# Optimization experiments

Measured on AMD Instinct MI355X. Metric: run time of the kernel, lower is better.

## Reference

```python
import jax, jax.numpy as jnp
import numpy as np

B, H, S, DK = 4, 16, 1024, 64


def setup_inputs() -> dict:
    key = jax.random.key(0)
    kq, kk, kv, km = jax.random.split(key, 4)
    q = jax.random.normal(kq, (B, H, S, DK), dtype=jnp.float32)
    k = jax.random.normal(kk, (B, H, S, DK), dtype=jnp.float32)
    v = jax.random.normal(kv, (B, H, S, DK), dtype=jnp.float32)
    mask = jax.random.randint(km, (B, 1, 1, S), 0, 2).astype(jnp.int32)
    return {"q": q, "k": k, "v": v, "mask": mask}


def reference(q, k, v, mask):
    dk = q.shape[-1]
    scale = 1.0 / np.sqrt(dk).astype(np.float32)
    # [B,H,S,S] scores
    qk = jnp.einsum("bhqd,bhkd->bhqk", q, k) * scale
    qk = jnp.where(mask == 0, jnp.float32(-10000.0), qk)
    attn_weight = jax.nn.softmax(qk, axis=-1)
    # NOTE: faithful to source bug — uses raw masked scores qk, not attn_weight
    output = jnp.einsum("bhqk,bhkd->bhqd", qk, v)
    return (output, attn_weight)
```

## Files before the change

### kernel.cpp

```cpp
#include <hip/hip_runtime.h>


typedef __attribute__((ext_vector_type(4))) float floatx4;
typedef __attribute__((ext_vector_type(8))) short shortx8;
typedef __attribute__((ext_vector_type(8))) unsigned short ushortx8;
typedef __attribute__((ext_vector_type(4))) int intx4;

#define S_ 1024
#define D_ 64
#define NELEM_ 4194304
#define ATTN_OFF 4194304
#define SCN 1040

__device__ __forceinline__ unsigned short f32_to_bf16(float f) {
    union { float f; unsigned u; } a; a.f = f;
    unsigned u = a.u;
    u += 0x7fffu + ((u >> 16) & 1u);
    return (unsigned short)(u >> 16);
}

__device__ __forceinline__ float bf16_to_f32(unsigned short h) {
    union { unsigned u; float f; } a; a.u = ((unsigned)h) << 16;
    return a.f;
}

__device__ __forceinline__ ushortx8 pack8u(floatx4 a, floatx4 b) {
    ushortx8 r;
    r[0] = f32_to_bf16(a[0]); r[1] = f32_to_bf16(a[1]);
    r[2] = f32_to_bf16(a[2]); r[3] = f32_to_bf16(a[3]);
    r[4] = f32_to_bf16(b[0]); r[5] = f32_to_bf16(b[1]);
    r[6] = f32_to_bf16(b[2]); r[7] = f32_to_bf16(b[3]);
    return r;
}

__global__ __launch_bounds__(256) void pack_kv(const float* __restrict__ k,
                                               const float* __restrict__ v,
                                               unsigned short* __restrict__ kbt,
                                               unsigned short* __restrict__ vtp) {
    __shared__ float tile[64][65];
    if (blockIdx.x < 1024) {
        int g = blockIdx.x * 256 + threadIdx.x;
        int lane = g & 63;
        int kt   = (g >> 6) & 63;
        int bh   = g >> 12;
        int quad = lane >> 4;
        int l15  = lane & 15;
        const float* src = k + ((size_t)(bh * S_ + kt * 16 + l15)) * D_ + quad * 8;
        floatx4 f0 = *(const floatx4*)(src);
        floatx4 f1 = *(const floatx4*)(src + 4);
        floatx4 f2 = *(const floatx4*)(src + 32);
        floatx4 f3 = *(const floatx4*)(src + 36);
        unsigned short* dst = kbt + (size_t)g * 16;
        *(ushortx8*)(dst)     = pack8u(f0, f1);
        *(ushortx8*)(dst + 8) = pack8u(f2, f3);
    } else {
        int blk = blockIdx.x - 1024;
        int bh = blk >> 4;
        int s0 = (blk & 15) << 6;
        int tid = threadIdx.x;
        int r  = tid >> 2;
        int c0 = (tid & 3) << 4;
        const float* src = v + ((size_t)(bh * S_ + s0 + r)) * D_ + c0;
        #pragma unroll
        for (int j = 0; j < 4; ++j) {
            floatx4 f = *(const floatx4*)(src + j * 4);
            tile[r][c0 + j*4 + 0] = f[0];
            tile[r][c0 + j*4 + 1] = f[1];
            tile[r][c0 + j*4 + 2] = f[2];
            tile[r][c0 + j*4 + 3] = f[3];
        }
        __syncthreads();
        int d  = tid >> 2;
        int so = (tid & 3) << 4;
        int dt  = d >> 4;
        int l15 = d & 15;
        ushortx8 h0, h1;
        #pragma unroll
        for (int j = 0; j < 8; ++j) h0[j] = f32_to_bf16(tile[so + j][d]);
        #pragma unroll
        for (int j = 0; j < 8; ++j) h1[j] = f32_to_bf16(tile[so + 8 + j][d]);
        int sA = s0 + so;
        int ksA = sA >> 5, qA = (sA & 31) >> 3;
        int sB = sA + 8;
        int ksB = sB >> 5, qB = (sB & 31) >> 3;
        size_t baseA = ((((size_t)bh * 4 + dt) * 32 + ksA) * 64 + qA * 16 + l15) * 8;
        size_t baseB = ((((size_t)bh * 4 + dt) * 32 + ksB) * 64 + qB * 16 + l15) * 8;
        *(ushortx8*)(vtp + baseA) = h0;
        *(ushortx8*)(vtp + baseB) = h1;
    }
}

__global__ __launch_bounds__(1024, 4) void attn_main(
    const float* __restrict__ q,
    const int* __restrict__ mask,
    const unsigned short* __restrict__ KbT,
    const unsigned short* __restrict__ VtP,
    float* __restrict__ out)
{
    __shared__ unsigned short sc[64 * SCN];
    __shared__ int msk[1024];

    int blk = blockIdx.x;
    int bh  = blk >> 4;
    int q0  = (blk & 15) << 6;
    int b   = bh >> 4;
    int tid = threadIdx.x;

    msk[tid] = mask[(b << 10) + tid];

    int w    = tid >> 6;
    int lane = tid & 63;
    int l15  = lane & 15;
    int quad = lane >> 4;
    int rg   = w & 3;
    int cg   = w >> 2;

    shortx8 qf0, qf1;
    {
        const float* qb = q + ((size_t)(bh * S_ + q0 + rg * 16 + l15)) * D_ + quad * 8;
        floatx4 a0 = *(const floatx4*)(qb);
        floatx4 a1 = *(const floatx4*)(qb + 4);
        floatx4 b0 = *(const floatx4*)(qb + 32);
        floatx4 b1 = *(const floatx4*)(qb + 36);
        ushortx8 u0 = pack8u(a0, a1);
        ushortx8 u1 = pack8u(b0, b1);
        qf0 = (shortx8)u0;
        qf1 = (shortx8)u1;
    }

    __syncthreads();

    {
        const unsigned short* kb = KbT + ((size_t)bh * 64 * 64 + lane) * 16;
        #pragma unroll 4
        for (int t = 0; t < 16; ++t) {
            int kt = (cg << 4) + t;
            const unsigned short* p = kb + (size_t)kt * (64 * 16);
            shortx8 kf0 = *(const shortx8*)(p);
            shortx8 kf1 = *(const shortx8*)(p + 8);
            floatx4 acc = {0.f, 0.f, 0.f, 0.f};
            acc = __builtin_amdgcn_mfma_f32_16x16x32_bf16(qf0, kf0, acc, 0, 0, 0);
            acc = __builtin_amdgcn_mfma_f32_16x16x32_bf16(qf1, kf1, acc, 0, 0, 0);
            int n0 = kt << 4;
            int mv = msk[n0 + l15];
            int col = n0 + l15;
            #pragma unroll
            for (int r = 0; r < 4; ++r) {
                unsigned short h = mv ? f32_to_bf16(acc[r] * 0.125f)
                                      : (unsigned short)0xC61C;
                sc[(rg * 16 + quad * 4 + r) * SCN + col] = h;
            }
        }
    }
    __syncthreads();

    auto phase2 = [&]() {
        float* attnb = out + ATTN_OFF + ((size_t)(bh * S_ + q0)) * S_;
        for (int rr = 0; rr < 4; ++rr) {
            int row = (w << 2) + rr;
            const unsigned short* srow = sc + row * SCN;
            float vv[16];
            #pragma unroll
            for (int c = 0; c < 2; ++c) {
                ushortx8 h = *(const ushortx8*)(srow + (c << 9) + lane * 8);
                #pragma unroll
                for (int j = 0; j < 8; ++j) vv[c * 8 + j] = bf16_to_f32(h[j]);
            }
            float m = vv[0];
            #pragma unroll
            for (int j = 1; j < 16; ++j) m = fmaxf(m, vv[j]);
            #pragma unroll
            for (int off = 32; off; off >>= 1) m = fmaxf(m, __shfl_xor(m, off));
            float s = 0.f;
            #pragma unroll
            for (int j = 0; j < 16; ++j) { vv[j] = __expf(vv[j] - m); s += vv[j]; }
            #pragma unroll
            for (int off = 32; off; off >>= 1) s += __shfl_xor(s, off);
            float inv = 1.0f / s;
            float* arow = attnb + (size_t)row * S_ + lane * 8;
            #pragma unroll
            for (int c = 0; c < 2; ++c) {
                floatx4 o0 = { vv[c*8+0]*inv, vv[c*8+1]*inv, vv[c*8+2]*inv, vv[c*8+3]*inv };
                floatx4 o1 = { vv[c*8+4]*inv, vv[c*8+5]*inv, vv[c*8+6]*inv, vv[c*8+7]*inv };
                *(floatx4*)(arow + (c << 9))     = o0;
                *(floatx4*)(arow + (c << 9) + 4) = o1;
            }
        }
    };
    auto phase3 = [&]() {
        const unsigned short* vb = VtP + (((size_t)bh * 4 + cg) * 32) * (64 * 8) + lane * 8;
        const unsigned short* sr = sc + (rg * 16 + l15) * SCN + quad * 8;
        floatx4 oacc = {0.f, 0.f, 0.f, 0.f};
        #pragma unroll 4
        for (int ks = 0; ks < 32; ++ks) {
            shortx8 af = *(const shortx8*)(sr + (ks << 5));
            shortx8 bf = *(const shortx8*)(vb + (ks << 9));
            oacc = __builtin_amdgcn_mfma_f32_16x16x32_bf16(af, bf, oacc, 0, 0, 0);
        }
        float* ob = out + ((size_t)(bh * S_ + q0 + rg * 16 + (quad << 2))) * D_
                        + (cg << 4) + l15;
        #pragma unroll
        for (int r = 0; r < 4; ++r) ob[(size_t)r * D_] = oacc[r];
    };
    if (w & 1) { phase3(); phase2(); }
    else       { phase2(); phase3(); }
}

extern "C" void kernel_launch(void* const* d_in, const int* in_sizes, int n_in,
                              void* d_out, int out_size, void* d_ws, size_t ws_size,
                              hipStream_t stream) {
    const float* q   = (const float*)d_in[0];
    const float* k   = (const float*)d_in[1];
    const float* v   = (const float*)d_in[2];
    const int* mask  = (const int*)d_in[3];
    float* out = (float*)d_out;
    unsigned short* KbT = (unsigned short*)d_ws;
    unsigned short* VtP = KbT + NELEM_;
    pack_kv<<<2048, 256, 0, stream>>>(k, v, KbT, VtP);
    attn_main<<<1024, 1024, 0, stream>>>(q, mask, KbT, VtP, out);
}
```

Before: 369.3 us.

## Reassign waves: register-blocked QK/PV tiles, dedicated softmax and PV waves, block swizzle

Each wave now holds all four Q row-group fragments and computes a 64x64 score block per K tile, so every K fragment load is reused across four MFMAs. The PV phase is handled by four dedicated waves that each reuse one V fragment across four row groups, while the other twelve waves do the softmax and attention-weight writes (6 or 5 rows each) instead of every wave doing both phases. It also pads the score row stride to change LDS bank mapping and swizzles the block index so consecutive blocks land on different heads. The costs are higher register pressure from the fragment and accumulator arrays, and an uneven split of work between the softmax waves and the PV waves.

Measured after the change: 387.6 us. +5.0%, slower.

```diff
diff --git a/kernel.cpp b/kernel.cpp
--- a/kernel.cpp
+++ b/kernel.cpp
@@ -4,13 +4,13 @@
 typedef __attribute__((ext_vector_type(4))) float floatx4;
 typedef __attribute__((ext_vector_type(8))) short shortx8;
 typedef __attribute__((ext_vector_type(8))) unsigned short ushortx8;
-typedef __attribute__((ext_vector_type(4))) int intx4;
 
 #define S_ 1024
 #define D_ 64
 #define NELEM_ 4194304
 #define ATTN_OFF 4194304
-#define SCN 1040
+#define SCN 1048
+#define QT 64
 
 __device__ __forceinline__ unsigned short f32_to_bf16(float f) {
     union { float f; unsigned u; } a; a.f = f;
@@ -97,10 +97,10 @@
     const unsigned short* __restrict__ VtP,
     float* __restrict__ out)
 {
-    __shared__ unsigned short sc[64 * SCN];
+    __shared__ unsigned short sc[QT * SCN];
     __shared__ int msk[1024];
 
-    int blk = blockIdx.x;
+    int blk = ((blockIdx.x & 7) << 7) | (blockIdx.x >> 3);
     int bh  = blk >> 4;
     int q0  = (blk & 15) << 6;
     int b   = bh >> 4;
@@ -112,52 +112,58 @@
     int lane = tid & 63;
     int l15  = lane & 15;
     int quad = lane >> 4;
-    int rg   = w & 3;
-    int cg   = w >> 2;
-
-    shortx8 qf0, qf1;
-    {
+
+    shortx8 qf0[4], qf1[4];
+    #pragma unroll
+    for (int rg = 0; rg < 4; ++rg) {
         const float* qb = q + ((size_t)(bh * S_ + q0 + rg * 16 + l15)) * D_ + quad * 8;
         floatx4 a0 = *(const floatx4*)(qb);
         floatx4 a1 = *(const floatx4*)(qb + 4);
-        floatx4 b0 = *(const floatx4*)(qb + 32);
-        floatx4 b1 = *(const floatx4*)(qb + 36);
-        ushortx8 u0 = pack8u(a0, a1);
-        ushortx8 u1 = pack8u(b0, b1);
-        qf0 = (shortx8)u0;
-        qf1 = (shortx8)u1;
+        floatx4 a2 = *(const floatx4*)(qb + 32);
+        floatx4 a3 = *(const floatx4*)(qb + 36);
+        qf0[rg] = (shortx8)pack8u(a0, a1);
+        qf1[rg] = (shortx8)pack8u(a2, a3);
     }
 
     __syncthreads();
 
     {
         const unsigned short* kb = KbT + ((size_t)bh * 64 * 64 + lane) * 16;
-        #pragma unroll 4
-        for (int t = 0; t < 16; ++t) {
-            int kt = (cg << 4) + t;
+        #pragma unroll
+        for (int t = 0; t < 4; ++t) {
+            int kt = (w << 2) + t;
             const unsigned short* p = kb + (size_t)kt * (64 * 16);
             shortx8 kf0 = *(const shortx8*)(p);
             shortx8 kf1 = *(const shortx8*)(p + 8);
-            floatx4 acc = {0.f, 0.f, 0.f, 0.f};
-            acc = __builtin_amdgcn_mfma_f32_16x16x32_bf16(qf0, kf0, acc, 0, 0, 0);
-            acc = __builtin_amdgcn_mfma_f32_16x16x32_bf16(qf1, kf1, acc, 0, 0, 0);
+            floatx4 acc[4];
+            #pragma unroll
+            for (int rg = 0; rg < 4; ++rg) {
+                acc[rg] = (floatx4){0.f, 0.f, 0.f, 0.f};
+                acc[rg] = __builtin_amdgcn_mfma_f32_16x16x32_bf16(qf0[rg], kf0, acc[rg], 0, 0, 0);
+                acc[rg] = __builtin_amdgcn_mfma_f32_16x16x32_bf16(qf1[rg], kf1, acc[rg], 0, 0, 0);
+            }
             int n0 = kt << 4;
             int mv = msk[n0 + l15];
             int col = n0 + l15;
             #pragma unroll
-            for (int r = 0; r < 4; ++r) {
-                unsigned short h = mv ? f32_to_bf16(acc[r] * 0.125f)
-                                      : (unsigned short)0xC61C;
-                sc[(rg * 16 + quad * 4 + r) * SCN + col] = h;
+            for (int rg = 0; rg < 4; ++rg) {
+                #pragma unroll
+                for (int r = 0; r < 4; ++r) {
+                    unsigned short h = mv ? f32_to_bf16(acc[rg][r] * 0.125f)
+                                          : (unsigned short)0xC61C;
+                    sc[(rg * 16 + quad * 4 + r) * SCN + col] = h;
+                }
             }
         }
     }
     __syncthreads();
 
-    auto phase2 = [&]() {
+    if (w < 12) {
+        int nrows = (w < 4) ? 6 : 5;
+        int row0  = (w < 4) ? w * 6 : 24 + (w - 4) * 5;
         float* attnb = out + ATTN_OFF + ((size_t)(bh * S_ + q0)) * S_;
-        for (int rr = 0; rr < 4; ++rr) {
-            int row = (w << 2) + rr;
+        for (int rr = 0; rr < nrows; ++rr) {
+            int row = row0 + rr;
             const unsigned short* srow = sc + row * SCN;
             float vv[16];
             #pragma unroll
@@ -186,24 +192,30 @@
                 *(floatx4*)(arow + (c << 9) + 4) = o1;
             }
         }
-    };
-    auto phase3 = [&]() {
+    } else {
+        int cg = w - 12;
         const unsigned short* vb = VtP + (((size_t)bh * 4 + cg) * 32) * (64 * 8) + lane * 8;
-        const unsigned short* sr = sc + (rg * 16 + l15) * SCN + quad * 8;
-        floatx4 oacc = {0.f, 0.f, 0.f, 0.f};
+        const unsigned short* srb = sc + l15 * SCN + quad * 8;
+        floatx4 oacc[4];
+        #pragma unroll
+        for (int rg = 0; rg < 4; ++rg) oacc[rg] = (floatx4){0.f, 0.f, 0.f, 0.f};
         #pragma unroll 4
         for (int ks = 0; ks < 32; ++ks) {
-            shortx8 af = *(const shortx8*)(sr + (ks << 5));
-            shortx8 bf = *(const shortx8*)(vb + (ks << 9));
-            oacc = __builtin_amdgcn_mfma_f32_16x16x32_bf16(af, bf, oacc, 0, 0, 0);
-        }
-        float* ob = out + ((size_t)(bh * S_ + q0 + rg * 16 + (quad << 2))) * D_
-                        + (cg << 4) + l15;
-        #pragma unroll
-        for (int r = 0; r < 4; ++r) ob[(size_t)r * D_] = oacc[r];
-    };
-    if (w & 1) { phase3(); phase2(); }
-    else       { phase2(); phase3(); }
+            shortx8 bfr = *(const shortx8*)(vb + (ks << 9));
+            #pragma unroll
+            for (int rg = 0; rg < 4; ++rg) {
+                shortx8 af = *(const shortx8*)(srb + (rg * 16) * SCN + (ks << 5));
+                oacc[rg] = __builtin_amdgcn_mfma_f32_16x16x32_bf16(af, bfr, oacc[rg], 0, 0, 0);
+            }
+        }
+        #pragma unroll
+        for (int rg = 0; rg < 4; ++rg) {
+            float* ob = out + ((size_t)(bh * S_ + q0 + rg * 16 + (quad << 2))) * D_
+                            + (cg << 4) + l15;
+            #pragma unroll
+            for (int r = 0; r < 4; ++r) ob[(size_t)r * D_] = oacc[rg][r];
+        }
+    }
 }
 
 extern "C" void kernel_launch(void* const* d_in, const int* in_sizes, int n_in,
```
